# Optimization experiments

Measured on AMD Instinct MI355X. Metric: run time of the kernel, lower is better.

## Reference

```python
import jax, jax.numpy as jnp
import numpy as np
import math

B, S, D = 16, 4096, 64

def setup_inputs() -> dict:
    key = jax.random.key(0)
    kq, kk, kv = jax.random.split(key, 3)
    query = jax.random.normal(kq, (B, S, D), dtype=jnp.float32)
    k_ = jax.random.normal(kk, (B, S, D), dtype=jnp.float32)
    value = jax.random.normal(kv, (B, S, D), dtype=jnp.float32)
    # causal mask: 1 = allowed, 0 = masked (set to -inf), broadcast over batch
    mask = jnp.tril(jnp.ones((S, S), dtype=jnp.int32))[None, :, :]
    return {"query": query, "key": k_, "value": value, "mask": mask, "key_dim": D}

def reference(query, key, value, mask, key_dim):
    # scores: [B, S, S] = Q @ K^T / sqrt(dk)
    scores = jnp.einsum('bqd,bkd->bqk', query, key) / math.sqrt(key_dim)
    scores = jnp.where(mask == 0, -jnp.inf, scores)
    attn = jax.nn.softmax(scores, axis=-1)
    return jnp.einsum('bqk,bkd->bqd', attn, value)
```

## Files before the change

kernel.cpp:

```cpp
#include <hip/hip_runtime.h>

typedef _Float16 half8 __attribute__((ext_vector_type(8)));
typedef float f32x4 __attribute__((ext_vector_type(4)));

union Frag { half8 v; unsigned int u32[4]; uint4 u4; };
union Pack4 { _Float16 h[4]; uint2 u; };

constexpr int S = 4096;
constexpr int D = 64;
constexpr int NB = 16;
constexpr int LTS = 72;

__global__ __launch_bounds__(256)
void prep_kernel(const float* __restrict__ K, const float* __restrict__ V,
                 _Float16* __restrict__ K16, _Float16* __restrict__ VT) {
    __shared__ float tl[64 * 66];
    const int tid = threadIdx.x;
    const int s0 = blockIdx.x * 64;
    const int b  = blockIdx.y;
    const float* Kb = K + ((size_t)b * S + s0) * D;
    const float* Vb = V + ((size_t)b * S + s0) * D;
    _Float16* K16b = K16 + ((size_t)b * S + s0) * D;

    #pragma unroll
    for (int i = 0; i < 2; ++i) {
        int e8 = tid + 256 * i;
        float4 a = ((const float4*)Kb)[2 * e8];
        float4 c = ((const float4*)Kb)[2 * e8 + 1];
        Frag f;
        f.v[0]=(_Float16)a.x; f.v[1]=(_Float16)a.y; f.v[2]=(_Float16)a.z; f.v[3]=(_Float16)a.w;
        f.v[4]=(_Float16)c.x; f.v[5]=(_Float16)c.y; f.v[6]=(_Float16)c.z; f.v[7]=(_Float16)c.w;
        ((uint4*)K16b)[e8] = f.u4;
    }
    #pragma unroll
    for (int i = 0; i < 4; ++i) {
        int fi = tid + 256 * i;
        int r = fi >> 4, c4 = (fi & 15) << 2;
        float4 v = *(const float4*)(Vb + (size_t)r * D + c4);
        float2* p = (float2*)&tl[r * 66 + c4];
        p[0] = make_float2(v.x, v.y);
        p[1] = make_float2(v.z, v.w);
    }
    __syncthreads();
    _Float16* VTb = VT + (size_t)b * D * S;
    #pragma unroll
    for (int i = 0; i < 2; ++i) {
        int fi = tid + 256 * i;
        int d = fi >> 3, s8 = (fi & 7) << 3;
        Frag f;
        #pragma unroll
        for (int j = 0; j < 8; ++j) f.v[j] = (_Float16)tl[(s8 + j) * 66 + d];
        *(uint4*)(VTb + (size_t)d * S + s0 + s8) = f.u4;
    }
}

template <int SPLIT>
__device__ __forceinline__
void fattn_body(const float* __restrict__ Q, const _Float16* __restrict__ K16,
                const _Float16* __restrict__ VT16, float* __restrict__ Out,
                float* __restrict__ OP, float* __restrict__ LP,
                int b, int J, int t0, int t1, int h) {
    __shared__ __align__(16) _Float16 kt[64 * LTS];
    __shared__ __align__(16) _Float16 vt[64 * LTS];
    __shared__ __align__(16) _Float16 pt[4 * 32 * LTS];

    const int tid  = threadIdx.x;
    const int wave = tid >> 6;
    const int lane = tid & 63;
    const int ln   = lane & 15;
    const int quad = lane >> 4;

    const float* Qb = Q + (size_t)b * S * D;
    const _Float16* Kb = K16 + (size_t)b * S * D;
    const _Float16* VTb = VT16 + (size_t)b * D * S;

    const float qscale = 0.125f * 1.44269504088896340736f;
    const int qrow_base = J * 128 + wave * 32;
    const int tw = (qrow_base + 31) >> 6;

    Frag qf[2][2];
    #pragma unroll
    for (int qg = 0; qg < 2; ++qg) {
        const float* qrow = Qb + (size_t)(qrow_base + qg * 16 + ln) * D + quad * 8;
        #pragma unroll
        for (int ks = 0; ks < 2; ++ks) {
            float4 a = *(const float4*)(qrow + ks * 32);
            float4 c = *(const float4*)(qrow + ks * 32 + 4);
            Frag f;
            f.v[0]=(_Float16)(a.x*qscale); f.v[1]=(_Float16)(a.y*qscale);
            f.v[2]=(_Float16)(a.z*qscale); f.v[3]=(_Float16)(a.w*qscale);
            f.v[4]=(_Float16)(c.x*qscale); f.v[5]=(_Float16)(c.y*qscale);
            f.v[6]=(_Float16)(c.z*qscale); f.v[7]=(_Float16)(c.w*qscale);
            qf[qg][ks] = f;
        }
    }

    f32x4 o[2][4] = {};
    float l_acc[2] = {0.f, 0.f};
    _Float16* ptw = pt + wave * 32 * LTS;

    for (int t = t0; t < t1; ++t) {
        const int k0 = t * 64;
        __syncthreads();

        #pragma unroll
        for (int i = 0; i < 2; ++i) {
            int fi = tid + 256 * i;
            int r = fi >> 3, c8 = (fi & 7) << 3;
            uint4 kk = *(const uint4*)(Kb + (size_t)(k0 + r) * D + c8);
            uint4 vv = *(const uint4*)(VTb + (size_t)r * S + k0 + c8);
            *(uint4*)(kt + r * LTS + c8) = kk;
            *(uint4*)(vt + r * LTS + c8) = vv;
        }
        __syncthreads();

        #pragma unroll
        for (int ct = 0; ct < 4; ++ct) {
            Frag kf0, kf1;
            kf0.u4 = *(const uint4*)(kt + (ct * 16 + ln) * LTS + quad * 8);
            kf1.u4 = *(const uint4*)(kt + (ct * 16 + ln) * LTS + 32 + quad * 8);
            #pragma unroll
            for (int qg = 0; qg < 2; ++qg) {
                f32x4 acc = {0.f, 0.f, 0.f, 0.f};
                acc = __builtin_amdgcn_mfma_f32_16x16x32_f16(kf0.v, qf[qg][0].v, acc, 0, 0, 0);
                acc = __builtin_amdgcn_mfma_f32_16x16x32_f16(kf1.v, qf[qg][1].v, acc, 0, 0, 0);
                if (t >= tw) {
                    int keyb = k0 + ct * 16 + quad * 4;
                    int qrow = qrow_base + qg * 16 + ln;
                    #pragma unroll
                    for (int r = 0; r < 4; ++r)
                        if (keyb + r > qrow) acc[r] = -1e30f;
                }
                Pack4 pk;
                float psum = 0.f;
                #pragma unroll
                for (int r = 0; r < 4; ++r) {
                    float p = exp2f(acc[r]);
                    psum += p;
                    pk.h[r] = (_Float16)p;
                }
                l_acc[qg] += psum;
                *(uint2*)(ptw + (qg * 16 + ln) * LTS + ct * 16 + quad * 4) = pk.u;
            }
        }

        Frag pf[2][2];
        #pragma unroll
        for (int qg = 0; qg < 2; ++qg)
            #pragma unroll
            for (int ks = 0; ks < 2; ++ks)
                pf[qg][ks].u4 = *(const uint4*)(ptw + (qg * 16 + ln) * LTS + ks * 32 + quad * 8);

        #pragma unroll
        for (int ks = 0; ks < 2; ++ks) {
            #pragma unroll
            for (int sub = 0; sub < 4; ++sub) {
                Frag vf;
                vf.u4 = *(const uint4*)(vt + (sub * 16 + ln) * LTS + ks * 32 + quad * 8);
                #pragma unroll
                for (int qg = 0; qg < 2; ++qg)
                    o[qg][sub] = __builtin_amdgcn_mfma_f32_16x16x32_f16(pf[qg][ks].v, vf.v, o[qg][sub], 0, 0, 0);
            }
        }
    }

    float lf[2];
    #pragma unroll
    for (int qg = 0; qg < 2; ++qg) {
        float x = l_acc[qg];
        x += __shfl_xor(x, 16, 64);
        x += __shfl_xor(x, 32, 64);
        lf[qg] = x;
    }

    if (SPLIT) {
        float* OPb = OP + (size_t)((b * 32 + J) * 2 + h) * 128 * 64;
        float* LPb = LP + (size_t)((b * 32 + J) * 2 + h) * 128;
        #pragma unroll
        for (int qg = 0; qg < 2; ++qg) {
            #pragma unroll
            for (int r = 0; r < 4; ++r)
                #pragma unroll
                for (int sub = 0; sub < 4; ++sub)
                    OPb[(wave * 32 + qg * 16 + quad * 4 + r) * 64 + sub * 16 + ln] = o[qg][sub][r];
            if (quad == 0) LPb[wave * 32 + qg * 16 + ln] = lf[qg];
        }
    } else {
        float* Ob = Out + (size_t)b * S * D;
        #pragma unroll
        for (int qg = 0; qg < 2; ++qg) {
            #pragma unroll
            for (int r = 0; r < 4; ++r) {
                float lrow = __shfl(lf[qg], quad * 4 + r, 64);
                float inv = 1.0f / lrow;
                #pragma unroll
                for (int sub = 0; sub < 4; ++sub)
                    Ob[(size_t)(qrow_base + qg * 16 + quad * 4 + r) * D + sub * 16 + ln] =
                        o[qg][sub][r] * inv;
            }
        }
    }
}

__global__ __launch_bounds__(256, 4)
void fattn_split_kernel(const float* __restrict__ Q, const _Float16* __restrict__ K16,
                        const _Float16* __restrict__ VT16,
                        float* __restrict__ OP, float* __restrict__ LP) {
    const int bx = blockIdx.x;
    const int J = 31 - (bx >> 5);
    const int h = (bx >> 4) & 1;
    const int b = bx & 15;
    const int n  = 2 * J + 2;
    const int n0 = (n + 1) >> 1;
    const int t0 = h ? n0 : 0;
    const int t1 = h ? n  : n0;
    fattn_body<1>(Q, K16, VT16, nullptr, OP, LP, b, J, t0, t1, h);
}

__global__ __launch_bounds__(256, 4)
void fattn_kernel(const float* __restrict__ Q, const _Float16* __restrict__ K16,
                  const _Float16* __restrict__ VT16, float* __restrict__ Out) {
    const int bx = blockIdx.x;
    const int J = 31 - (bx >> 4);
    const int b = bx & 15;
    fattn_body<0>(Q, K16, VT16, Out, nullptr, nullptr, b, J, 0, 2 * J + 2, 0);
}

__global__ __launch_bounds__(256)
void reduce_kernel(const float* __restrict__ OP, const float* __restrict__ LP,
                   float* __restrict__ Out) {
    const int rb = blockIdx.x;
    const int b  = rb & 15;
    const int J  = rb >> 4;
    const int tid = threadIdx.x;
    const float* p0 = OP + (size_t)((b * 32 + J) * 2) * 8192;
    const float* p1 = p0 + 8192;
    const float* l0 = LP + (size_t)((b * 32 + J) * 2) * 128;
    const float* l1 = l0 + 128;
    float* Ob = Out + (size_t)b * S * D + (size_t)J * 8192;
    #pragma unroll
    for (int i = 0; i < 8; ++i) {
        int e4 = tid + 256 * i;
        float4 a = ((const float4*)p0)[e4];
        float4 c = ((const float4*)p1)[e4];
        int q = e4 >> 4;
        float inv = 1.0f / (l0[q] + l1[q]);
        float4 r;
        r.x = (a.x + c.x) * inv;
        r.y = (a.y + c.y) * inv;
        r.z = (a.z + c.z) * inv;
        r.w = (a.w + c.w) * inv;
        ((float4*)Ob)[e4] = r;
    }
}

extern "C" void kernel_launch(void* const* d_in, const int* in_sizes, int n_in,
                              void* d_out, int out_size, void* d_ws, size_t ws_size,
                              hipStream_t stream) {
    const float* Q = (const float*)d_in[0];
    const float* K = (const float*)d_in[1];
    const float* V = (const float*)d_in[2];
    float* O = (float*)d_out;

    const size_t prepBytes = (size_t)NB * S * D * 2;
    _Float16* K16  = (_Float16*)d_ws;
    _Float16* VT16 = (_Float16*)((char*)d_ws + prepBytes);

    const size_t opOff = 2 * prepBytes;
    const size_t opBytes = (size_t)NB * 32 * 2 * 128 * 64 * 4;
    const size_t lpOff = opOff + opBytes;
    const size_t lpBytes = (size_t)NB * 32 * 2 * 128 * 4;
    const size_t need = lpOff + lpBytes;

    hipLaunchKernelGGL(prep_kernel, dim3(S / 64, NB), dim3(256), 0, stream, K, V, K16, VT16);

    if (ws_size >= need) {
        float* OP = (float*)((char*)d_ws + opOff);
        float* LP = (float*)((char*)d_ws + lpOff);
        hipLaunchKernelGGL(fattn_split_kernel, dim3(64 * NB), dim3(256), 0, stream,
                           Q, K16, VT16, OP, LP);
        hipLaunchKernelGGL(reduce_kernel, dim3(32 * NB), dim3(256), 0, stream, OP, LP, O);
    } else {
        hipLaunchKernelGGL(fattn_kernel, dim3(32 * NB), dim3(256), 0, stream, Q, K16, VT16, O);
    }
}
```

Before: 203.4 us.

## Split causal attention KV range four ways with fp16 normalized partials

Raises the KV split from 2 to 4 chunks per query block, launching twice as many attention blocks so work is spread more evenly over the GPU's compute units. Each partial output is now normalized by its own row sum and stored as fp16, which halves partial-output traffic; the reduce kernel recombines the chunks weighted by their row sums. This relies on the shared fixed max (no running-max rescale) being consistent across splits. In exchange it adds more blocks and a larger reduce, and fp16 partials lose some precision.

Measured after the change: 200.3 us. No clear change (-1.6%).

```diff
diff --git a/kernel.cpp b/kernel.cpp
--- a/kernel.cpp
+++ b/kernel.cpp
@@ -58,7 +58,7 @@
 __device__ __forceinline__
 void fattn_body(const float* __restrict__ Q, const _Float16* __restrict__ K16,
                 const _Float16* __restrict__ VT16, float* __restrict__ Out,
-                float* __restrict__ OP, float* __restrict__ LP,
+                _Float16* __restrict__ OP, float* __restrict__ LP,
                 int b, int J, int t0, int t1, int h) {
     __shared__ __align__(16) _Float16 kt[64 * LTS];
     __shared__ __align__(16) _Float16 vt[64 * LTS];
@@ -174,16 +174,20 @@
     }
 
     if (SPLIT) {
-        float* OPb = OP + (size_t)((b * 32 + J) * 2 + h) * 128 * 64;
-        float* LPb = LP + (size_t)((b * 32 + J) * 2 + h) * 128;
+        _Float16* OPb = OP + (size_t)(((b * 32 + J) * 4 + h)) * 8192;
+        float* LPb = LP + (size_t)(((b * 32 + J) * 4 + h)) * 128;
         #pragma unroll
         for (int qg = 0; qg < 2; ++qg) {
-            #pragma unroll
-            for (int r = 0; r < 4; ++r)
+            if (quad == 0) LPb[wave * 32 + qg * 16 + ln] = lf[qg];
+            #pragma unroll
+            for (int r = 0; r < 4; ++r) {
+                float lrow = __shfl(lf[qg], quad * 4 + r, 64);
+                float inv = (lrow > 0.f) ? (1.0f / lrow) : 0.f;
                 #pragma unroll
                 for (int sub = 0; sub < 4; ++sub)
-                    OPb[(wave * 32 + qg * 16 + quad * 4 + r) * 64 + sub * 16 + ln] = o[qg][sub][r];
-            if (quad == 0) LPb[wave * 32 + qg * 16 + ln] = lf[qg];
+                    OPb[(wave * 32 + qg * 16 + quad * 4 + r) * 64 + sub * 16 + ln] =
+                        (_Float16)(o[qg][sub][r] * inv);
+            }
         }
     } else {
         float* Ob = Out + (size_t)b * S * D;
@@ -205,15 +209,14 @@
 __global__ __launch_bounds__(256, 4)
 void fattn_split_kernel(const float* __restrict__ Q, const _Float16* __restrict__ K16,
                         const _Float16* __restrict__ VT16,
-                        float* __restrict__ OP, float* __restrict__ LP) {
+                        _Float16* __restrict__ OP, float* __restrict__ LP) {
     const int bx = blockIdx.x;
-    const int J = 31 - (bx >> 5);
-    const int h = (bx >> 4) & 1;
+    const int J = 31 - (bx >> 6);
+    const int h = (bx >> 4) & 3;
     const int b = bx & 15;
     const int n  = 2 * J + 2;
-    const int n0 = (n + 1) >> 1;
-    const int t0 = h ? n0 : 0;
-    const int t1 = h ? n  : n0;
+    const int t0 = (h * n) >> 2;
+    const int t1 = ((h + 1) * n) >> 2;
     fattn_body<1>(Q, K16, VT16, nullptr, OP, LP, b, J, t0, t1, h);
 }
 
@@ -227,30 +230,35 @@
 }
 
 __global__ __launch_bounds__(256)
-void reduce_kernel(const float* __restrict__ OP, const float* __restrict__ LP,
+void reduce_kernel(const _Float16* __restrict__ OP, const float* __restrict__ LP,
                    float* __restrict__ Out) {
     const int rb = blockIdx.x;
     const int b  = rb & 15;
     const int J  = rb >> 4;
     const int tid = threadIdx.x;
-    const float* p0 = OP + (size_t)((b * 32 + J) * 2) * 8192;
-    const float* p1 = p0 + 8192;
-    const float* l0 = LP + (size_t)((b * 32 + J) * 2) * 128;
-    const float* l1 = l0 + 128;
+    const _Float16* p = OP + (size_t)(b * 32 + J) * 4 * 8192;
+    const float* l = LP + (size_t)(b * 32 + J) * 4 * 128;
     float* Ob = Out + (size_t)b * S * D + (size_t)J * 8192;
     #pragma unroll
-    for (int i = 0; i < 8; ++i) {
-        int e4 = tid + 256 * i;
-        float4 a = ((const float4*)p0)[e4];
-        float4 c = ((const float4*)p1)[e4];
-        int q = e4 >> 4;
-        float inv = 1.0f / (l0[q] + l1[q]);
-        float4 r;
-        r.x = (a.x + c.x) * inv;
-        r.y = (a.y + c.y) * inv;
-        r.z = (a.z + c.z) * inv;
-        r.w = (a.w + c.w) * inv;
-        ((float4*)Ob)[e4] = r;
+    for (int i = 0; i < 4; ++i) {
+        int e8 = tid + 256 * i;
+        int q  = e8 >> 3;
+        float lw[4], lsum = 0.f;
+        #pragma unroll
+        for (int hh = 0; hh < 4; ++hh) { lw[hh] = l[hh * 128 + q]; lsum += lw[hh]; }
+        float inv = 1.0f / lsum;
+        float acc[8] = {};
+        #pragma unroll
+        for (int hh = 0; hh < 4; ++hh) {
+            half8 v = *(const half8*)(p + (size_t)hh * 8192 + e8 * 8);
+            #pragma unroll
+            for (int j = 0; j < 8; ++j) acc[j] += lw[hh] * (float)v[j];
+        }
+        float4 r0, r1;
+        r0.x = acc[0]*inv; r0.y = acc[1]*inv; r0.z = acc[2]*inv; r0.w = acc[3]*inv;
+        r1.x = acc[4]*inv; r1.y = acc[5]*inv; r1.z = acc[6]*inv; r1.w = acc[7]*inv;
+        ((float4*)Ob)[2 * e8]     = r0;
+        ((float4*)Ob)[2 * e8 + 1] = r1;
     }
 }
 
@@ -267,17 +275,17 @@
     _Float16* VT16 = (_Float16*)((char*)d_ws + prepBytes);
 
     const size_t opOff = 2 * prepBytes;
-    const size_t opBytes = (size_t)NB * 32 * 2 * 128 * 64 * 4;
+    const size_t opBytes = (size_t)NB * 32 * 4 * 8192 * 2;
     const size_t lpOff = opOff + opBytes;
-    const size_t lpBytes = (size_t)NB * 32 * 2 * 128 * 4;
+    const size_t lpBytes = (size_t)NB * 32 * 4 * 128 * 4;
     const size_t need = lpOff + lpBytes;
 
     hipLaunchKernelGGL(prep_kernel, dim3(S / 64, NB), dim3(256), 0, stream, K, V, K16, VT16);
 
     if (ws_size >= need) {
-        float* OP = (float*)((char*)d_ws + opOff);
+        _Float16* OP = (_Float16*)((char*)d_ws + opOff);
         float* LP = (float*)((char*)d_ws + lpOff);
-        hipLaunchKernelGGL(fattn_split_kernel, dim3(64 * NB), dim3(256), 0, stream,
+        hipLaunchKernelGGL(fattn_split_kernel, dim3(128 * NB), dim3(256), 0, stream,
                            Q, K16, VT16, OP, LP);
         hipLaunchKernelGGL(reduce_kernel, dim3(32 * NB), dim3(256), 0, stream, OP, LP, O);
     } else {
```
